# Optimization experiments

Measured on AMD Instinct MI355X. Metric: run time of the kernel, lower is better.

## Reference

```python
import jax, jax.numpy as jnp
import numpy as np

ALPHA = 0.25
GAMMA = 2.0
CONSTRAINT_WEIGHT = 2.0
EPOCH = 0  # current_epoch default


def _smooth_l1(s):
    # F.smooth_l1_loss(s, ones) elementwise, beta=1.0
    d = s - 1.0
    ad = jnp.abs(d)
    return jnp.where(ad < 1.0, 0.5 * d * d, ad - 0.5)


def setup_inputs() -> dict:
    key = jax.random.key(0)
    k1, k2 = jax.random.split(key)
    B = 131072
    outputs = jax.random.normal(k1, (B, 81, 9), dtype=jnp.float32)
    targets = jax.random.randint(k2, (B, 81), 0, 9, dtype=jnp.int64)
    return {"outputs": outputs, "targets": targets}


def reference(outputs, targets):
    B = outputs.shape[0]
    logits = outputs.reshape(B, 81, 9)
    logp = jax.nn.log_softmax(logits, axis=-1)          # [B,81,9]
    tgt = targets.reshape(B, 81)
    # per-cell cross entropy
    ce = -jnp.take_along_axis(logp, tgt[..., None], axis=-1)[..., 0]  # [B,81]
    pt = jnp.exp(-ce)
    focal_loss = jnp.mean(ALPHA * (1.0 - pt) ** GAMMA * ce)

    probs = jnp.exp(logp).reshape(B, 9, 9, 9)           # [B,row,col,digit]
    row_sums = probs.sum(axis=2)                        # [B,row,digit]
    col_sums = probs.sum(axis=1)                        # [B,col,digit]
    box_sums = probs.reshape(B, 3, 3, 3, 3, 9).sum(axis=(2, 4)).reshape(B, 9, 9)
    # sum over 9 digits of per-digit means == 9 * mean over all elements
    constraint_loss = 9.0 * (jnp.mean(_smooth_l1(row_sums))
                             + jnp.mean(_smooth_l1(col_sums))
                             + jnp.mean(_smooth_l1(box_sums)))
    constraint_loss = constraint_loss / 27.0

    epoch_factor = min(1.0, EPOCH / 50)
    dyn_w = CONSTRAINT_WEIGHT * (0.5 + 0.5 * epoch_factor)
    return focal_loss + dyn_w * constraint_loss
```

## Files before the change

### kernel.cpp

```cpp
#include <hip/hip_runtime.h>
#include <hip/hip_bf16.h>


constexpr int BLOCK = 256;
constexpr int WPB = 4;
constexpr float ALPHA = 0.25f;

__global__ __launch_bounds__(BLOCK) void focal_constraint_main(
    const float* __restrict__ outs,
    const int* __restrict__ tgts,
    double* __restrict__ acc,
    int B)
{
    __shared__ float probs[WPB][736];
    __shared__ float red[WPB];

    const int lane = threadIdx.x & 63;
    const int wave = threadIdx.x >> 6;
    const int gw = blockIdx.x * WPB + wave;
    const int nwaves = gridDim.x * WPB;

    float* P = probs[wave];
    float lacc = 0.0f;

    const int iters = (B + nwaves - 1) / nwaves;
    for (int it = 0; it < iters; ++it) {
        const int s = gw + it * nwaves;
        const bool active = (s < B);

        if (active) {
            const float* __restrict__ src = outs + (size_t)s * 729;
            const int* __restrict__ tg = tgts + (size_t)s * 81;
            #pragma unroll
            for (int cc = 0; cc < 2; ++cc) {
                const int cell = lane + cc * 64;
                if (cell < 81) {
                    float v[9];
                    #pragma unroll
                    for (int d = 0; d < 9; ++d) v[d] = src[cell * 9 + d];
                    float m = v[0];
                    #pragma unroll
                    for (int d = 1; d < 9; ++d) m = fmaxf(m, v[d]);
                    float e[9];
                    float sum = 0.0f;
                    #pragma unroll
                    for (int d = 0; d < 9; ++d) { e[d] = __expf(v[d] - m); sum += e[d]; }
                    const float inv = 1.0f / sum;
                    #pragma unroll
                    for (int d = 0; d < 9; ++d) P[cell * 9 + d] = e[d] * inv;
                    const int t = tg[cell];
                    const float ce = __logf(sum) - (v[t] - m);
                    const float pt = e[t] * inv;
                    const float om = 1.0f - pt;
                    lacc += ALPHA * om * om * ce;
                }
            }
        }
        __syncthreads();

        if (active) {
            #pragma unroll
            for (int k = 0; k < 4; ++k) {
                const int idx = lane + k * 64;
                if (idx < 243) {
                    const int grp = idx / 81;
                    const int t2 = idx - grp * 81;
                    const int a = t2 / 9;
                    const int d = t2 - a * 9;
                    float ssum = 0.0f;
                    if (grp == 0) {
                        #pragma unroll
                        for (int c = 0; c < 9; ++c) ssum += P[(a * 9 + c) * 9 + d];
                    } else if (grp == 1) {
                        #pragma unroll
                        for (int r = 0; r < 9; ++r) ssum += P[(r * 9 + a) * 9 + d];
                    } else {
                        const int br = (a / 3) * 3, bc = (a % 3) * 3;
                        #pragma unroll
                        for (int i = 0; i < 3; ++i)
                            #pragma unroll
                            for (int j = 0; j < 3; ++j)
                                ssum += P[((br + i) * 9 + (bc + j)) * 9 + d];
                    }
                    const float dd = ssum - 1.0f;
                    const float ad = fabsf(dd);
                    const float sl1 = (ad < 1.0f) ? 0.5f * dd * dd : ad - 0.5f;
                    lacc += sl1 * (1.0f / 3.0f);
                }
            }
        }
        __syncthreads();
    }

    #pragma unroll
    for (int off = 32; off > 0; off >>= 1) lacc += __shfl_xor(lacc, off, 64);
    if (lane == 0) red[wave] = lacc;
    __syncthreads();
    if (threadIdx.x == 0) {
        double bsum = 0.0;
        #pragma unroll
        for (int w = 0; w < WPB; ++w) bsum += (double)red[w];
        atomicAdd(acc, bsum);
    }
}

__global__ void focal_constraint_finalize(const double* __restrict__ acc,
                                          float* __restrict__ out,
                                          double scale)
{
    out[0] = (float)(acc[0] * scale);
}

extern "C" void kernel_launch(void* const* d_in, const int* in_sizes, int n_in,
                              void* d_out, int out_size, void* d_ws, size_t ws_size,
                              hipStream_t stream) {
    const float* outs = (const float*)d_in[0];
    const int* tgts = (const int*)d_in[1];
    const int B = in_sizes[0] / 729;

    double* acc = (double*)d_ws;
    hipMemsetAsync(acc, 0, sizeof(double), stream);

    const int grid = 2048;
    focal_constraint_main<<<grid, BLOCK, 0, stream>>>(outs, tgts, acc, B);

    const double scale = 1.0 / ((double)B * 81.0);
    focal_constraint_finalize<<<1, 1, 0, stream>>>(acc, (float*)d_out, scale);
}
```

Baseline: 534.2 us.

## Stage block's four samples into LDS with coalesced float4 loads

Each block now loads four consecutive samples (2916 floats plus 324 targets) into shared memory with coalesced float4 and int4 loads. Softmax then reads logits from LDS, where before each lane made strided 9-float global reads. This targets poor coalescing of the 36-byte-stride per-cell loads. It assumes B is divisible by 4 and the buffers are 16-byte aligned, and it adds a barrier per group with no overlap between loading and compute.

```diff
diff --git a/kernel.cpp b/kernel.cpp
--- a/kernel.cpp
+++ b/kernel.cpp
@@ -10,83 +10,86 @@
     const float* __restrict__ outs,
     const int* __restrict__ tgts,
     double* __restrict__ acc,
-    int B)
+    int ngroups)
 {
-    __shared__ float probs[WPB][736];
+    __shared__ float P[WPB * 729];
+    __shared__ int   T[WPB * 81];
     __shared__ float red[WPB];
 
     const int lane = threadIdx.x & 63;
     const int wave = threadIdx.x >> 6;
-    const int gw = blockIdx.x * WPB + wave;
-    const int nwaves = gridDim.x * WPB;
 
-    float* P = probs[wave];
     float lacc = 0.0f;
 
-    const int iters = (B + nwaves - 1) / nwaves;
-    for (int it = 0; it < iters; ++it) {
-        const int s = gw + it * nwaves;
-        const bool active = (s < B);
+    for (int g = blockIdx.x; g < ngroups; g += gridDim.x) {
+        const float4* __restrict__ src4 =
+            reinterpret_cast<const float4*>(outs + (size_t)g * (WPB * 729));
+        #pragma unroll
+        for (int r = 0; r < 3; ++r) {
+            const int idx = threadIdx.x + r * BLOCK;
+            if (idx < 729) reinterpret_cast<float4*>(P)[idx] = src4[idx];
+        }
+        if (threadIdx.x < (WPB * 81) / 4) {
+            reinterpret_cast<int4*>(T)[threadIdx.x] =
+                reinterpret_cast<const int4*>(tgts + (size_t)g * (WPB * 81))[threadIdx.x];
+        }
+        __syncthreads();
 
-        if (active) {
-            const float* __restrict__ src = outs + (size_t)s * 729;
-            const int* __restrict__ tg = tgts + (size_t)s * 81;
-            #pragma unroll
-            for (int cc = 0; cc < 2; ++cc) {
-                const int cell = lane + cc * 64;
-                if (cell < 81) {
-                    float v[9];
-                    #pragma unroll
-                    for (int d = 0; d < 9; ++d) v[d] = src[cell * 9 + d];
-                    float m = v[0];
-                    #pragma unroll
-                    for (int d = 1; d < 9; ++d) m = fmaxf(m, v[d]);
-                    float e[9];
-                    float sum = 0.0f;
-                    #pragma unroll
-                    for (int d = 0; d < 9; ++d) { e[d] = __expf(v[d] - m); sum += e[d]; }
-                    const float inv = 1.0f / sum;
-                    #pragma unroll
-                    for (int d = 0; d < 9; ++d) P[cell * 9 + d] = e[d] * inv;
-                    const int t = tg[cell];
-                    const float ce = __logf(sum) - (v[t] - m);
-                    const float pt = e[t] * inv;
-                    const float om = 1.0f - pt;
-                    lacc += ALPHA * om * om * ce;
-                }
+        float* __restrict__ Ps = P + wave * 729;
+        const int* __restrict__ Ts = T + wave * 81;
+        #pragma unroll
+        for (int cc = 0; cc < 2; ++cc) {
+            const int cell = lane + cc * 64;
+            if (cell < 81) {
+                float v[9];
+                #pragma unroll
+                for (int d = 0; d < 9; ++d) v[d] = Ps[cell * 9 + d];
+                float m = v[0];
+                #pragma unroll
+                for (int d = 1; d < 9; ++d) m = fmaxf(m, v[d]);
+                float e[9];
+                float sum = 0.0f;
+                #pragma unroll
+                for (int d = 0; d < 9; ++d) { e[d] = __expf(v[d] - m); sum += e[d]; }
+                const float inv = 1.0f / sum;
+                #pragma unroll
+                for (int d = 0; d < 9; ++d) Ps[cell * 9 + d] = e[d] * inv;
+                const int t = Ts[cell];
+                const float ce = __logf(sum) - (v[t] - m);
+                const float pt = e[t] * inv;
+                const float om = 1.0f - pt;
+                lacc += ALPHA * om * om * ce;
             }
         }
         __syncthreads();
 
-        if (active) {
-            #pragma unroll
-            for (int k = 0; k < 4; ++k) {
-                const int idx = lane + k * 64;
-                if (idx < 243) {
-                    const int grp = idx / 81;
-                    const int t2 = idx - grp * 81;
-                    const int a = t2 / 9;
-                    const int d = t2 - a * 9;
-                    float ssum = 0.0f;
-                    if (grp == 0) {
+        #pragma unroll
+        for (int k = 0; k < 4; ++k) {
+            const int idx = lane + k * 64;
+            if (idx < 243) {
+                const int grp = idx / 81;
+                const int t2 = idx - grp * 81;
+                const int a = t2 / 9;
+                const int d = t2 - a * 9;
+                float ssum = 0.0f;
+                if (grp == 0) {
+                    #pragma unroll
+                    for (int c = 0; c < 9; ++c) ssum += Ps[(a * 9 + c) * 9 + d];
+                } else if (grp == 1) {
+                    #pragma unroll
+                    for (int r = 0; r < 9; ++r) ssum += Ps[(r * 9 + a) * 9 + d];
+                } else {
+                    const int br = (a / 3) * 3, bc = (a % 3) * 3;
+                    #pragma unroll
+                    for (int i = 0; i < 3; ++i)
                         #pragma unroll
-                        for (int c = 0; c < 9; ++c) ssum += P[(a * 9 + c) * 9 + d];
-                    } else if (grp == 1) {
-                        #pragma unroll
-                        for (int r = 0; r < 9; ++r) ssum += P[(r * 9 + a) * 9 + d];
-                    } else {
-                        const int br = (a / 3) * 3, bc = (a % 3) * 3;
-                        #pragma unroll
-                        for (int i = 0; i < 3; ++i)
-                            #pragma unroll
-                            for (int j = 0; j < 3; ++j)
-                                ssum += P[((br + i) * 9 + (bc + j)) * 9 + d];
-                    }
-                    const float dd = ssum - 1.0f;
-                    const float ad = fabsf(dd);
-                    const float sl1 = (ad < 1.0f) ? 0.5f * dd * dd : ad - 0.5f;
-                    lacc += sl1 * (1.0f / 3.0f);
+                        for (int j = 0; j < 3; ++j)
+                            ssum += Ps[((br + i) * 9 + (bc + j)) * 9 + d];
                 }
+                const float dd = ssum - 1.0f;
+                const float ad = fabsf(dd);
+                const float sl1 = (ad < 1.0f) ? 0.5f * dd * dd : ad - 0.5f;
+                lacc += sl1 * (1.0f / 3.0f);
             }
         }
         __syncthreads();
@@ -117,12 +120,14 @@
     const float* outs = (const float*)d_in[0];
     const int* tgts = (const int*)d_in[1];
     const int B = in_sizes[0] / 729;
+    const int ngroups = B / WPB;
 
     double* acc = (double*)d_ws;
     hipMemsetAsync(acc, 0, sizeof(double), stream);
 
-    const int grid = 2048;
-    focal_constraint_main<<<grid, BLOCK, 0, stream>>>(outs, tgts, acc, B);
+    int grid = 2048;
+    if (grid > ngroups) grid = ngroups;
+    focal_constraint_main<<<grid, BLOCK, 0, stream>>>(outs, tgts, acc, ngroups);
 
     const double scale = 1.0 / ((double)B * 81.0);
     focal_constraint_finalize<<<1, 1, 0, stream>>>(acc, (float*)d_out, scale);
```

After: 533.8 us. No clear change (-0.1%).
